# Performance work log

Hardware: AMD Instinct MI355X
Metric: run time of the kernel (lower is better)

## Reference

```python
import jax, jax.numpy as jnp
import numpy as np

# Irreps: in1 = in2 = out = 8x0e + 8x1o  (mul_ir / e3nn layout: [scalars(8) | vectors(8,3)])
MUL = 8
DIM = 4 * MUL           # 8*1 + 8*3 = 32
NPATH = 4               # (0e,0e->0e), (1o,1o->0e), (0e,1o->1o), (1o,0e->1o)
WNUM = NPATH * MUL**3   # 2048
BATCH = 1 << 20

# Real O3 Clebsch-Gordan values (component normalization, e3nn convention):
#   C(0e,0e->0e) = 1 ;  C(1o,1o->0e)_ij = delta_ij / sqrt(3)
#   C(0e,1o->1o)_jk = delta_jk ;  C(1o,0e->1o)_ik = delta_ik
INV_SQRT3 = 1.0 / np.sqrt(3.0)
# Path normalization: each output irrep receives 2 paths with fan-in mul*mul each
ALPHA = 1.0 / np.sqrt(2.0 * MUL * MUL)


def setup_inputs() -> dict:
    key = jax.random.key(0)
    k1, k2, k3 = jax.random.split(key, 3)
    x1 = jax.random.normal(k1, (BATCH, DIM), dtype=jnp.float32)
    x2 = jax.random.normal(k2, (BATCH, DIM), dtype=jnp.float32)
    weight = jax.random.normal(k3, (1, WNUM), dtype=jnp.float32)
    return {"x1": x1, "x2": x2, "weight": weight}


def reference(x1, x2, weight):
    B = x1.shape[0]
    n = MUL ** 3
    w = weight[0]
    # per-path fully-connected weights, each (mul1, mul2, mul3)
    W0 = w[0 * n:1 * n].reshape(MUL, MUL, MUL)  # 0e x 0e -> 0e
    W1 = w[1 * n:2 * n].reshape(MUL, MUL, MUL)  # 1o x 1o -> 0e
    W2 = w[2 * n:3 * n].reshape(MUL, MUL, MUL)  # 0e x 1o -> 1o
    W3 = w[3 * n:4 * n].reshape(MUL, MUL, MUL)  # 1o x 0e -> 1o

    s1 = x1[:, :MUL]                       # (B, 8) scalars
    v1 = x1[:, MUL:].reshape(B, MUL, 3)    # (B, 8, 3) vectors
    s2 = x2[:, :MUL]
    v2 = x2[:, MUL:].reshape(B, MUL, 3)

    # 0e output: scalar*scalar path + vector-dot path (CG = delta_ij/sqrt(3))
    out0 = (jnp.einsum('bu,bv,uvw->bw', s1, s2, W0)
            + INV_SQRT3 * jnp.einsum('bui,bvi,uvw->bw', v1, v2, W1))
    # 1o output: scalar*vector paths (CG = identity on the vector index)
    out1 = (jnp.einsum('bu,bvk,uvw->bwk', s1, v2, W2)
            + jnp.einsum('buk,bv,uvw->bwk', v1, s2, W3))

    out = jnp.concatenate([out0, out1.reshape(B, 3 * MUL)], axis=-1)
    return ALPHA * out
```

## Files before the change

kernel.cpp:

```cpp
#include <hip/hip_runtime.h>


typedef float v2f __attribute__((ext_vector_type(2)));

constexpr int TPB = 256;

__global__ __launch_bounds__(TPB) void tp_kernel(
    const float* __restrict__ x1,
    const float* __restrict__ x2,
    const float* __restrict__ wg,
    float* __restrict__ out,
    int batch)
{
    const float INV3  = 0.57735026918962576f;
    const float ALPHA = 0.088388347648318447f;

    int b = blockIdx.x * TPB + threadIdx.x;
    if (b >= batch) return;

    float X1[32], X2[32];
    {
        const float4* p1 = (const float4*)(x1 + (size_t)b * 32);
        const float4* p2 = (const float4*)(x2 + (size_t)b * 32);
        #pragma unroll
        for (int j = 0; j < 8; ++j) {
            float4 t1 = p1[j];
            X1[4*j+0] = t1.x; X1[4*j+1] = t1.y; X1[4*j+2] = t1.z; X1[4*j+3] = t1.w;
            float4 t2 = p2[j];
            X2[4*j+0] = t2.x; X2[4*j+1] = t2.y; X2[4*j+2] = t2.z; X2[4*j+3] = t2.w;
        }
    }

    v2f acc0[4], acc0b[4], a01[8];
    float a2[8];
    #pragma unroll
    for (int j = 0; j < 4; ++j) { acc0[j] = (v2f){0.f,0.f}; acc0b[j] = (v2f){0.f,0.f}; }
    #pragma unroll
    for (int t = 0; t < 8; ++t) { a01[t] = (v2f){0.f,0.f}; a2[t] = 0.f; }

    #pragma unroll
    for (int v = 0; v < 8; ++v) {
        float s2v = X2[v];
        float c0 = X2[8+v*3+0], c1 = X2[8+v*3+1], c2 = X2[8+v*3+2];
        v2f cc01 = {c0, c1};
        v2f e[4] = {{0.f,0.f},{0.f,0.f},{0.f,0.f},{0.f,0.f}};

        #pragma unroll
        for (int u = 0; u < 8; ++u) {
            float s1u = X1[u];
            float p = s1u * s2v;
            float d = X1[8+u*3+0]*c0 + X1[8+u*3+1]*c1 + X1[8+u*3+2]*c2;
            v2f pp = {p, p}, dd = {d, d}, ss = {s1u, s1u};
            const v2f* w0 = (const v2f*)(wg +         u*64 + v*8);
            const v2f* w1 = (const v2f*)(wg +  512 +  u*64 + v*8);
            const v2f* w2 = (const v2f*)(wg + 1024 +  u*64 + v*8);
            #pragma unroll
            for (int j = 0; j < 4; ++j) {
                acc0[j]  = __builtin_elementwise_fma(pp, w0[j], acc0[j]);
                acc0b[j] = __builtin_elementwise_fma(dd, w1[j], acc0b[j]);
                e[j]     = __builtin_elementwise_fma(ss, w2[j], e[j]);
            }
        }
        #pragma unroll
        for (int j = 0; j < 4; ++j) {
            float e0 = e[j].x, e1 = e[j].y;
            v2f ee0 = {e0, e0}, ee1 = {e1, e1};
            a01[2*j]   = __builtin_elementwise_fma(cc01, ee0, a01[2*j]);
            a01[2*j+1] = __builtin_elementwise_fma(cc01, ee1, a01[2*j+1]);
            a2[2*j]   += c2 * e0;
            a2[2*j+1] += c2 * e1;
        }
    }

    #pragma unroll
    for (int u = 0; u < 8; ++u) {
        v2f f[4] = {{0.f,0.f},{0.f,0.f},{0.f,0.f},{0.f,0.f}};
        #pragma unroll
        for (int v = 0; v < 8; ++v) {
            float sv = X2[v];
            v2f ss = {sv, sv};
            const v2f* w3 = (const v2f*)(wg + 1536 + u*64 + v*8);
            #pragma unroll
            for (int j = 0; j < 4; ++j)
                f[j] = __builtin_elementwise_fma(ss, w3[j], f[j]);
        }
        float c0 = X1[8+u*3+0], c1 = X1[8+u*3+1], c2 = X1[8+u*3+2];
        v2f cc01 = {c0, c1};
        #pragma unroll
        for (int j = 0; j < 4; ++j) {
            float f0 = f[j].x, f1 = f[j].y;
            v2f ff0 = {f0, f0}, ff1 = {f1, f1};
            a01[2*j]   = __builtin_elementwise_fma(cc01, ff0, a01[2*j]);
            a01[2*j+1] = __builtin_elementwise_fma(cc01, ff1, a01[2*j+1]);
            a2[2*j]   += c2 * f0;
            a2[2*j+1] += c2 * f1;
        }
    }

    float O[32];
    #pragma unroll
    for (int j = 0; j < 4; ++j) {
        v2f iv = {INV3, INV3}, al = {ALPHA, ALPHA};
        v2f o = al * (acc0[j] + iv * acc0b[j]);
        O[2*j]   = o.x;
        O[2*j+1] = o.y;
    }
    #pragma unroll
    for (int t = 0; t < 8; ++t) {
        O[8 + t*3 + 0] = ALPHA * a01[t].x;
        O[8 + t*3 + 1] = ALPHA * a01[t].y;
        O[8 + t*3 + 2] = ALPHA * a2[t];
    }
    float4* po = (float4*)(out + (size_t)b * 32);
    #pragma unroll
    for (int j = 0; j < 8; ++j) {
        po[j] = make_float4(O[4*j+0], O[4*j+1], O[4*j+2], O[4*j+3]);
    }
}

extern "C" void kernel_launch(void* const* d_in, const int* in_sizes, int n_in,
                              void* d_out, int out_size, void* d_ws, size_t ws_size,
                              hipStream_t stream) {
    const float* x1 = (const float*)d_in[0];
    const float* x2 = (const float*)d_in[1];
    const float* wg = (const float*)d_in[2];
    float* out = (float*)d_out;

    int batch = in_sizes[0] / 32;
    dim3 grid((batch + TPB - 1) / TPB), block(TPB);
    hipLaunchKernelGGL(tp_kernel, grid, block, 0, stream, x1, x2, wg, out, batch);
}
```

Measured before the change: 369.3 us.

## Split contraction into phases to cut register pressure and raise occupancy

Restructures the per-thread computation into separate phases: the scalar output is computed first (with the 1/sqrt(3) folded into x2 vectors and both paths merged into one accumulator) and stored early, then the vector outputs. x2 vectors are re-loaded from global memory in halves instead of kept live. Launch bounds request 6 waves per SIMD, and stores become nontemporal. The aim is fewer live registers and higher occupancy, at the cost of re-reading x2 and possible spills under the tighter register cap.

After: 741.7 us. 101% more time.

```diff
diff --git a/kernel.cpp b/kernel.cpp
--- a/kernel.cpp
+++ b/kernel.cpp
@@ -2,10 +2,11 @@
 
 
 typedef float v2f __attribute__((ext_vector_type(2)));
+typedef float v4f __attribute__((ext_vector_type(4)));
 
 constexpr int TPB = 256;
 
-__global__ __launch_bounds__(TPB) void tp_kernel(
+__global__ __launch_bounds__(TPB, 6) void tp_kernel(
     const float* __restrict__ x1,
     const float* __restrict__ x2,
     const float* __restrict__ wg,
@@ -18,73 +19,96 @@
     int b = blockIdx.x * TPB + threadIdx.x;
     if (b >= batch) return;
 
-    float X1[32], X2[32];
+    const float* r1 = x1 + (size_t)b * 32;
+    const float* r2 = x2 + (size_t)b * 32;
+    float*       ro = out + (size_t)b * 32;
+
+    float s1[8], s2[8], V1[24];
     {
-        const float4* p1 = (const float4*)(x1 + (size_t)b * 32);
-        const float4* p2 = (const float4*)(x2 + (size_t)b * 32);
+        const v4f* p1 = (const v4f*)r1;
+        const v4f* p2 = (const v4f*)r2;
         #pragma unroll
-        for (int j = 0; j < 8; ++j) {
-            float4 t1 = p1[j];
-            X1[4*j+0] = t1.x; X1[4*j+1] = t1.y; X1[4*j+2] = t1.z; X1[4*j+3] = t1.w;
-            float4 t2 = p2[j];
-            X2[4*j+0] = t2.x; X2[4*j+1] = t2.y; X2[4*j+2] = t2.z; X2[4*j+3] = t2.w;
+        for (int j = 0; j < 2; ++j) {
+            v4f t1 = p1[j], t2 = p2[j];
+            #pragma unroll
+            for (int i = 0; i < 4; ++i) { s1[4*j+i] = t1[i]; s2[4*j+i] = t2[i]; }
+        }
+        #pragma unroll
+        for (int j = 0; j < 6; ++j) {
+            v4f t = p1[2+j];
+            #pragma unroll
+            for (int i = 0; i < 4; ++i) V1[4*j+i] = t[i];
         }
     }
 
-    v2f acc0[4], acc0b[4], a01[8];
-    float a2[8];
+    v2f acc0[4];
     #pragma unroll
-    for (int j = 0; j < 4; ++j) { acc0[j] = (v2f){0.f,0.f}; acc0b[j] = (v2f){0.f,0.f}; }
-    #pragma unroll
-    for (int t = 0; t < 8; ++t) { a01[t] = (v2f){0.f,0.f}; a2[t] = 0.f; }
+    for (int j = 0; j < 4; ++j) acc0[j] = (v2f){0.f, 0.f};
 
     #pragma unroll
-    for (int v = 0; v < 8; ++v) {
-        float s2v = X2[v];
-        float c0 = X2[8+v*3+0], c1 = X2[8+v*3+1], c2 = X2[8+v*3+2];
-        v2f cc01 = {c0, c1};
-        v2f e[4] = {{0.f,0.f},{0.f,0.f},{0.f,0.f},{0.f,0.f}};
-
-        #pragma unroll
-        for (int u = 0; u < 8; ++u) {
-            float s1u = X1[u];
-            float p = s1u * s2v;
-            float d = X1[8+u*3+0]*c0 + X1[8+u*3+1]*c1 + X1[8+u*3+2]*c2;
-            v2f pp = {p, p}, dd = {d, d}, ss = {s1u, s1u};
-            const v2f* w0 = (const v2f*)(wg +         u*64 + v*8);
-            const v2f* w1 = (const v2f*)(wg +  512 +  u*64 + v*8);
-            const v2f* w2 = (const v2f*)(wg + 1024 +  u*64 + v*8);
+    for (int h = 0; h < 2; ++h) {
+        float C[12];
+        {
+            const v4f* pv = (const v4f*)(r2 + 8 + 12*h);
             #pragma unroll
-            for (int j = 0; j < 4; ++j) {
-                acc0[j]  = __builtin_elementwise_fma(pp, w0[j], acc0[j]);
-                acc0b[j] = __builtin_elementwise_fma(dd, w1[j], acc0b[j]);
-                e[j]     = __builtin_elementwise_fma(ss, w2[j], e[j]);
+            for (int j = 0; j < 3; ++j) {
+                v4f t = pv[j];
+                #pragma unroll
+                for (int i = 0; i < 4; ++i) C[4*j+i] = t[i] * INV3;
             }
         }
         #pragma unroll
-        for (int j = 0; j < 4; ++j) {
-            float e0 = e[j].x, e1 = e[j].y;
-            v2f ee0 = {e0, e0}, ee1 = {e1, e1};
-            a01[2*j]   = __builtin_elementwise_fma(cc01, ee0, a01[2*j]);
-            a01[2*j+1] = __builtin_elementwise_fma(cc01, ee1, a01[2*j+1]);
-            a2[2*j]   += c2 * e0;
-            a2[2*j+1] += c2 * e1;
+        for (int vv = 0; vv < 4; ++vv) {
+            const int v = 4*h + vv;
+            float s2v = s2[v];
+            float c0 = C[3*vv+0], c1 = C[3*vv+1], c2 = C[3*vv+2];
+            #pragma unroll
+            for (int u = 0; u < 8; ++u) {
+                float p = s1[u] * s2v;
+                float d = V1[3*u+0]*c0 + V1[3*u+1]*c1 + V1[3*u+2]*c2;
+                v2f pp = {p, p}, dd = {d, d};
+                const v2f* w0 = (const v2f*)(wg +        u*64 + v*8);
+                const v2f* w1 = (const v2f*)(wg + 512 +  u*64 + v*8);
+                #pragma unroll
+                for (int j = 0; j < 4; ++j) {
+                    acc0[j] = __builtin_elementwise_fma(pp, w0[j], acc0[j]);
+                    acc0[j] = __builtin_elementwise_fma(dd, w1[j], acc0[j]);
+                }
+            }
         }
     }
 
+    {
+        v4f o0, o1;
+        o0[0] = ALPHA * acc0[0].x; o0[1] = ALPHA * acc0[0].y;
+        o0[2] = ALPHA * acc0[1].x; o0[3] = ALPHA * acc0[1].y;
+        o1[0] = ALPHA * acc0[2].x; o1[1] = ALPHA * acc0[2].y;
+        o1[2] = ALPHA * acc0[3].x; o1[3] = ALPHA * acc0[3].y;
+        __builtin_nontemporal_store(o0, (v4f*)ro);
+        __builtin_nontemporal_store(o1, (v4f*)ro + 1);
+    }
+
+    asm volatile("" ::: "memory");
+
+    v2f a01[8]; float a2[8];
+    #pragma unroll
+    for (int t = 0; t < 8; ++t) { a01[t] = (v2f){0.f, 0.f}; a2[t] = 0.f; }
+
     #pragma unroll
     for (int u = 0; u < 8; ++u) {
-        v2f f[4] = {{0.f,0.f},{0.f,0.f},{0.f,0.f},{0.f,0.f}};
+        v2f f[4];
+        #pragma unroll
+        for (int j = 0; j < 4; ++j) f[j] = (v2f){0.f, 0.f};
         #pragma unroll
         for (int v = 0; v < 8; ++v) {
-            float sv = X2[v];
+            float sv = s2[v];
             v2f ss = {sv, sv};
             const v2f* w3 = (const v2f*)(wg + 1536 + u*64 + v*8);
             #pragma unroll
             for (int j = 0; j < 4; ++j)
                 f[j] = __builtin_elementwise_fma(ss, w3[j], f[j]);
         }
-        float c0 = X1[8+u*3+0], c1 = X1[8+u*3+1], c2 = X1[8+u*3+2];
+        float c0 = V1[3*u+0], c1 = V1[3*u+1], c2 = V1[3*u+2];
         v2f cc01 = {c0, c1};
         #pragma unroll
         for (int j = 0; j < 4; ++j) {
@@ -97,24 +121,58 @@
         }
     }
 
-    float O[32];
     #pragma unroll
-    for (int j = 0; j < 4; ++j) {
-        v2f iv = {INV3, INV3}, al = {ALPHA, ALPHA};
-        v2f o = al * (acc0[j] + iv * acc0b[j]);
-        O[2*j]   = o.x;
-        O[2*j+1] = o.y;
+    for (int h = 0; h < 2; ++h) {
+        float C[12];
+        {
+            const v4f* pv = (const v4f*)(r2 + 8 + 12*h);
+            #pragma unroll
+            for (int j = 0; j < 3; ++j) {
+                v4f t = pv[j];
+                #pragma unroll
+                for (int i = 0; i < 4; ++i) C[4*j+i] = t[i];
+            }
+        }
+        #pragma unroll
+        for (int vv = 0; vv < 4; ++vv) {
+            const int v = 4*h + vv;
+            v2f e[4];
+            #pragma unroll
+            for (int j = 0; j < 4; ++j) e[j] = (v2f){0.f, 0.f};
+            #pragma unroll
+            for (int u = 0; u < 8; ++u) {
+                v2f ss = {s1[u], s1[u]};
+                const v2f* w2 = (const v2f*)(wg + 1024 + u*64 + v*8);
+                #pragma unroll
+                for (int j = 0; j < 4; ++j)
+                    e[j] = __builtin_elementwise_fma(ss, w2[j], e[j]);
+            }
+            float c0 = C[3*vv+0], c1 = C[3*vv+1], c2 = C[3*vv+2];
+            v2f cc01 = {c0, c1};
+            #pragma unroll
+            for (int j = 0; j < 4; ++j) {
+                float e0 = e[j].x, e1 = e[j].y;
+                v2f ee0 = {e0, e0}, ee1 = {e1, e1};
+                a01[2*j]   = __builtin_elementwise_fma(cc01, ee0, a01[2*j]);
+                a01[2*j+1] = __builtin_elementwise_fma(cc01, ee1, a01[2*j+1]);
+                a2[2*j]   += c2 * e0;
+                a2[2*j+1] += c2 * e1;
+            }
+        }
+    }
+
+    float O[24];
+    #pragma unroll
+    for (int t = 0; t < 8; ++t) {
+        O[3*t+0] = ALPHA * a01[t].x;
+        O[3*t+1] = ALPHA * a01[t].y;
+        O[3*t+2] = ALPHA * a2[t];
     }
     #pragma unroll
-    for (int t = 0; t < 8; ++t) {
-        O[8 + t*3 + 0] = ALPHA * a01[t].x;
-        O[8 + t*3 + 1] = ALPHA * a01[t].y;
-        O[8 + t*3 + 2] = ALPHA * a2[t];
-    }
-    float4* po = (float4*)(out + (size_t)b * 32);
-    #pragma unroll
-    for (int j = 0; j < 8; ++j) {
-        po[j] = make_float4(O[4*j+0], O[4*j+1], O[4*j+2], O[4*j+3]);
+    for (int j = 0; j < 6; ++j) {
+        v4f t;
+        t[0] = O[4*j+0]; t[1] = O[4*j+1]; t[2] = O[4*j+2]; t[3] = O[4*j+3];
+        __builtin_nontemporal_store(t, (v4f*)(ro + 8) + j);
     }
 }
 
```
